# Optimization experiments

Measured on AMD Instinct MI355X. Metric: run time of the kernel, lower is better.

The kernel has to match this reference:

```python
import jax, jax.numpy as jnp
import numpy as np

KERNEL_MUL = 2.0
KERNEL_NUM = 5
EPS = 1e-3


def setup_inputs() -> dict:
    key = jax.random.key(0)
    k1, k2 = jax.random.split(key)
    source = jax.random.normal(k1, (2048, 512), dtype=jnp.float32)
    target = jax.random.normal(k2, (2048, 512), dtype=jnp.float32)
    beta = jnp.ones((KERNEL_NUM,), dtype=jnp.float32) / KERNEL_NUM
    return {"source": source, "target": target, "beta": beta}


def _sq_dists(total):
    # squared Euclidean pairwise distances, (N, N), clamped >= 0 (matches cdist(p=2)**2)
    sq = jnp.sum(total * total, axis=-1)
    d = sq[:, None] + sq[None, :] - 2.0 * (total @ total.T)
    return jnp.maximum(d, 0.0)


def _project_simplex(v):
    m = v.shape[0]
    mu = -jnp.sort(-v)                      # descending
    cs = jnp.cumsum(mu)
    ar = jnp.arange(1, m + 1, dtype=v.dtype)
    cond = mu - (cs - 1.0) / ar > 0
    idx = jnp.where(cond, jnp.arange(m), -1)
    rho = jnp.where(jnp.any(cond), jnp.max(idx), 0)
    theta = (cs[rho] - 1.0) / (rho + 1).astype(v.dtype)
    p = jnp.maximum(v - theta, 0.0)
    return p / (p.sum() + 1e-12)


def _update_beta(source, target, beta):
    # Batched version of the per-pair quad-kernel loop in _update_beta.
    Ns, D = source.shape
    Nt = target.shape[0]
    P = min(Ns // 2, Nt // 2)  # num_effective_pairs (static)
    s = source[: 2 * P].reshape(P, 2, D)
    t = target[: 2 * P].reshape(P, 2, D)
    quad = jnp.concatenate([s, t], axis=1)              # (P, 4, D) -> [s1, s2, t1, t2]
    diff = quad[:, :, None, :] - quad[:, None, :, :]
    sq = jnp.sum(diff * diff, axis=-1)                  # (P, 4, 4)
    offdiag = ~np.eye(4, dtype=bool)
    bw = jnp.median(sq[:, offdiag], axis=1) + 1e-6      # per-pair median of nonzero dists
    bw = bw / (KERNEL_MUL ** (KERNEL_NUM // 2))
    bws = bw[:, None] * (KERNEL_MUL ** jnp.arange(KERNEL_NUM, dtype=bw.dtype))[None, :]
    K = jnp.exp(-sq[:, None, :, :] / bws[:, :, None, None])   # (P, 5, 4, 4)
    g = K[:, :, 0, 1] + K[:, :, 2, 3] - K[:, :, 0, 2] - K[:, :, 1, 3]  # (P, 5)
    gm = jnp.mean(g, axis=0)
    Q = (g.T @ g) / P - jnp.outer(gm, gm) + EPS * jnp.eye(KERNEL_NUM, dtype=g.dtype)
    # projected gradient descent on the simplex (lr=1, max_iter=100, tol=1e-6)
    def cond_fn(st):
        _, _, i, conv = st
        return (i < 100) & (~conv)
    def body_fn(st):
        b, _, i, _ = st
        proj = _project_simplex(b - Q @ b)
        conv = jnp.linalg.norm(proj - b) < 1e-6
        return (proj, proj, i + 1, conv)
    _, proj, _, _ = jax.lax.while_loop(
        cond_fn, body_fn, (beta, beta, jnp.int32(0), jnp.array(False)))
    return proj


def _forward(source, target, beta):
    beta_new = _update_beta(jax.lax.stop_gradient(source),
                            jax.lax.stop_gradient(target), beta)
    Ns = source.shape[0]
    total = jnp.concatenate([source, target], axis=0)   # (N, D)
    N = total.shape[0]
    sq = _sq_dists(total)                               # (N, N)
    offdiag = ~np.eye(N, dtype=bool)
    bw = jnp.median(sq[offdiag]) + 1e-6
    bw = bw / (KERNEL_MUL ** (KERNEL_NUM // 2))
    bws = bw * (KERNEL_MUL ** jnp.arange(KERNEL_NUM, dtype=sq.dtype))  # (5,)
    Ks = jnp.exp(-sq[None, :, :] / bws[:, None, None])  # (5, N, N)
    joint = jnp.einsum('k,kij->ij', beta_new, Ks)
    XX = joint[:Ns, :Ns]
    YY = joint[Ns:, Ns:]
    XY = joint[:Ns, Ns:]
    n = XX.shape[0]
    m = YY.shape[0]
    term_XX = (jnp.sum(XX) - jnp.trace(XX)) / (n * (n - 1))
    term_YY = (jnp.sum(YY) - jnp.trace(YY)) / (m * (m - 1))
    term_XY = jnp.sum(XY) / (n * m)
    loss = term_XX + term_YY - 2.0 * term_XY
    return jnp.maximum(loss, 0.0)


def reference(source, target, beta):
    return _forward(source, target, beta)
```

## Files before the change

### kernel.cpp

```cpp
#include <hip/hip_runtime.h>
#include <math.h>

#define NT 4096
#define NS 2048
#define DDIM 512
#define KN 5
#define NTILES 528

typedef __bf16 bf16x8 __attribute__((ext_vector_type(8)));
typedef float f32x4 __attribute__((ext_vector_type(4)));
typedef unsigned short u16x8 __attribute__((ext_vector_type(8)));

static __device__ inline unsigned short f2bf(float x) {
    unsigned u = __float_as_uint(x);
    unsigned r = (u + 0x7fffu + ((u >> 16) & 1u)) >> 16;
    return (unsigned short)r;
}
static __device__ inline float bf2f(unsigned short h) {
    return __uint_as_float(((unsigned)h) << 16);
}

static __device__ inline void tri_map(int b, int& bx, int& by) {
    int x = (int)((sqrtf(8.0f * (float)b + 1.0f) - 1.0f) * 0.5f);
    while ((x + 1) * (x + 2) / 2 <= b) ++x;
    while (x * (x + 1) / 2 > b) --x;
    bx = x;
    by = b - x * (x + 1) / 2;
}

static __device__ void beta_solve(const float* __restrict__ g,
                                  const float* __restrict__ beta_in,
                                  float* __restrict__ beta_out)
{
    int lane = threadIdx.x;
    float gs[KN] = {0, 0, 0, 0, 0};
    float gg[15];
    #pragma unroll
    for (int i = 0; i < 15; ++i) gg[i] = 0.0f;
    for (int p = lane; p < 1024; p += 64) {
        float gv[KN];
        #pragma unroll
        for (int k = 0; k < KN; ++k) gv[k] = g[(size_t)p * KN + k];
        int idx = 0;
        #pragma unroll
        for (int a2 = 0; a2 < KN; ++a2) {
            gs[a2] += gv[a2];
            #pragma unroll
            for (int b2 = a2; b2 < KN; ++b2) gg[idx++] += gv[a2] * gv[b2];
        }
    }
    #pragma unroll
    for (int m = 32; m > 0; m >>= 1) {
        #pragma unroll
        for (int k = 0; k < KN; ++k) gs[k] += __shfl_xor(gs[k], m);
        #pragma unroll
        for (int i = 0; i < 15; ++i) gg[i] += __shfl_xor(gg[i], m);
    }
    if (lane != 0) return;

    float Q[KN][KN], gm[KN];
    #pragma unroll
    for (int k = 0; k < KN; ++k) gm[k] = gs[k] * (1.0f / 1024.0f);
    int idx = 0;
    #pragma unroll
    for (int a2 = 0; a2 < KN; ++a2)
        #pragma unroll
        for (int b2 = a2; b2 < KN; ++b2) {
            float qv = gg[idx++] * (1.0f / 1024.0f) - gm[a2] * gm[b2];
            Q[a2][b2] = qv; Q[b2][a2] = qv;
        }
    #pragma unroll
    for (int k = 0; k < KN; ++k) Q[k][k] += 0.001f;

    float b[KN], proj[KN];
    #pragma unroll
    for (int k = 0; k < KN; ++k) { b[k] = beta_in[k]; proj[k] = b[k]; }
    for (int it = 0; it < 100; ++it) {
        float v[KN];
        #pragma unroll
        for (int a2 = 0; a2 < KN; ++a2) {
            float qb = Q[a2][0] * b[0] + Q[a2][1] * b[1] + Q[a2][2] * b[2]
                     + Q[a2][3] * b[3] + Q[a2][4] * b[4];
            v[a2] = b[a2] - qb;
        }
        float mu0 = v[0], mu1 = v[1], mu2 = v[2], mu3 = v[3], mu4 = v[4];
#define CMPSW(x, y) { float hi_ = fmaxf(x, y); float lo_ = fminf(x, y); x = hi_; y = lo_; }
        CMPSW(mu0, mu1) CMPSW(mu3, mu4) CMPSW(mu2, mu4) CMPSW(mu2, mu3)
        CMPSW(mu0, mu3) CMPSW(mu0, mu2) CMPSW(mu1, mu4) CMPSW(mu1, mu3) CMPSW(mu1, mu2)
#undef CMPSW
        float cs0 = mu0, cs1 = cs0 + mu1, cs2 = cs1 + mu2, cs3 = cs2 + mu3, cs4 = cs3 + mu4;
        bool c1 = mu1 * 2.0f > cs1 - 1.0f;
        bool c2 = mu2 * 3.0f > cs2 - 1.0f;
        bool c3 = mu3 * 4.0f > cs3 - 1.0f;
        bool c4 = mu4 * 5.0f > cs4 - 1.0f;
        float csSel = cs0, rcpSel = 1.0f;
        if (c1) { csSel = cs1; rcpSel = 0.5f; }
        if (c2) { csSel = cs2; rcpSel = (1.0f / 3.0f); }
        if (c3) { csSel = cs3; rcpSel = 0.25f; }
        if (c4) { csSel = cs4; rcpSel = 0.2f; }
        float theta = (csSel - 1.0f) * rcpSel;
        float ssum = 0.0f;
        #pragma unroll
        for (int k = 0; k < KN; ++k) { proj[k] = fmaxf(v[k] - theta, 0.0f); ssum += proj[k]; }
        float invs = 1.0f / (ssum + 1e-12f);
        float nd = 0.0f;
        #pragma unroll
        for (int k = 0; k < KN; ++k) {
            proj[k] *= invs;
            float dd = proj[k] - b[k];
            nd += dd * dd;
            b[k] = proj[k];
        }
        if (nd < 1e-12f) break;
    }
    #pragma unroll
    for (int k = 0; k < KN; ++k) beta_out[k] = proj[k];
}

#define NZERO (4096 + 64 + 64 + 65536 + 65536)
__global__ __launch_bounds__(256) void k_prep2(const float* __restrict__ S,
                                               const float* __restrict__ T,
                                               unsigned short* __restrict__ Hi,
                                               unsigned short* __restrict__ Lo,
                                               float* __restrict__ norms,
                                               float* __restrict__ g,
                                               unsigned* __restrict__ hists,
                                               unsigned* __restrict__ sel)
{
    for (unsigned i = blockIdx.x * 256 + threadIdx.x; i < NZERO; i += 65536) hists[i] = 0;
    if (blockIdx.x == 50 && threadIdx.x == 0) {
        sel[0] = 0u; sel[1] = 8386559u;
        sel[2] = 0u; sel[3] = 8386560u;
    }
    int p = blockIdx.x * 4 + (threadIdx.x >> 6);
    int l = threadIdx.x & 63;
    const float* r0 = S + (size_t)(2 * p) * DDIM;
    const float* r1 = r0 + DDIM;
    const float* r2 = T + (size_t)(2 * p) * DDIM;
    const float* r3 = r2 + DDIM;
    float a[8], b[8], c[8], d[8];
    *(float4*)&a[0] = *(const float4*)(r0 + l * 8); *(float4*)&a[4] = *(const float4*)(r0 + l * 8 + 4);
    *(float4*)&b[0] = *(const float4*)(r1 + l * 8); *(float4*)&b[4] = *(const float4*)(r1 + l * 8 + 4);
    *(float4*)&c[0] = *(const float4*)(r2 + l * 8); *(float4*)&c[4] = *(const float4*)(r2 + l * 8 + 4);
    *(float4*)&d[0] = *(const float4*)(r3 + l * 8); *(float4*)&d[4] = *(const float4*)(r3 + l * 8 + 4);

    float n0 = 0, n1 = 0, n2 = 0, n3 = 0;
    float s01 = 0, s23 = 0, s02 = 0, s13 = 0, s03 = 0, s12 = 0;
    u16x8 h0, l0, h1, l1, h2, l2, h3, l3;
    #pragma unroll
    for (int k = 0; k < 8; ++k) {
        float va = a[k], vb = b[k], vc = c[k], vd = d[k];
        n0 += va * va; n1 += vb * vb; n2 += vc * vc; n3 += vd * vd;
        float t01 = va - vb, t23 = vc - vd, t02 = va - vc, t13 = vb - vd;
        s01 += t01*t01; s23 += t23*t23; s02 += t02*t02; s13 += t13*t13;
        float t03 = va - vd, t12 = vb - vc;
        s03 += t03*t03; s12 += t12*t12;
        unsigned short hh;
        hh = f2bf(va); h0[k] = hh; l0[k] = f2bf(va - bf2f(hh));
        hh = f2bf(vb); h1[k] = hh; l1[k] = f2bf(vb - bf2f(hh));
        hh = f2bf(vc); h2[k] = hh; l2[k] = f2bf(vc - bf2f(hh));
        hh = f2bf(vd); h3[k] = hh; l3[k] = f2bf(vd - bf2f(hh));
    }
    size_t g0 = (size_t)(2 * p) * DDIM + l * 8;
    size_t g1 = g0 + DDIM;
    size_t g2 = (size_t)(NS + 2 * p) * DDIM + l * 8;
    size_t g3 = g2 + DDIM;
    *(u16x8*)&Hi[g0] = h0; *(u16x8*)&Lo[g0] = l0;
    *(u16x8*)&Hi[g1] = h1; *(u16x8*)&Lo[g1] = l1;
    *(u16x8*)&Hi[g2] = h2; *(u16x8*)&Lo[g2] = l2;
    *(u16x8*)&Hi[g3] = h3; *(u16x8*)&Lo[g3] = l3;

    #pragma unroll
    for (int m = 32; m > 0; m >>= 1) {
        n0 += __shfl_xor(n0, m); n1 += __shfl_xor(n1, m);
        n2 += __shfl_xor(n2, m); n3 += __shfl_xor(n3, m);
        s01 += __shfl_xor(s01, m); s23 += __shfl_xor(s23, m);
        s02 += __shfl_xor(s02, m); s13 += __shfl_xor(s13, m);
        s03 += __shfl_xor(s03, m); s12 += __shfl_xor(s12, m);
    }
    if (l == 0) {
        norms[2 * p] = n0; norms[2 * p + 1] = n1;
        norms[NS + 2 * p] = n2; norms[NS + 2 * p + 1] = n3;
        float v[6] = { s01, s02, s03, s12, s13, s23 };
        for (int i = 0; i < 5; ++i)
            for (int j = 0; j < 5 - i; ++j)
                if (v[j] > v[j + 1]) { float t = v[j]; v[j] = v[j + 1]; v[j + 1] = t; }
        float med = 0.5f * (v[2] + v[3]);
        float bw = (med + 1e-6f) * 0.25f;
        #pragma unroll
        for (int k = 0; k < KN; ++k) {
            float inv = 1.0f / (bw * (float)(1 << k));
            g[(size_t)p * KN + k] = expf(-s01 * inv) + expf(-s23 * inv)
                                  - expf(-s02 * inv) - expf(-s13 * inv);
        }
    }
}

__global__ __launch_bounds__(256) void k_dist_mfma(const unsigned short* __restrict__ Hi,
                                                   const unsigned short* __restrict__ Lo,
                                                   const float* __restrict__ norms,
                                                   float* __restrict__ D,
                                                   unsigned short* __restrict__ D16,
                                                   int do16,
                                                   const float* __restrict__ g,
                                                   const float* __restrict__ beta_in,
                                                   float* __restrict__ beta_out)
{
    __shared__ __align__(16) unsigned short sA[2][2][128][32];
    __shared__ __align__(16) unsigned short sB[2][2][128][32];

    if (blockIdx.x == 0) {
        if (threadIdx.x < 64) beta_solve(g, beta_in, beta_out);
        return;
    }

    int bb = blockIdx.x - 1;
    int swz = (bb & 7) * 66 + (bb >> 3);
    int bx, by;
    tri_map(swz, bx, by);
    const int m0 = by * 128, n0 = bx * 128;

    const int tid = threadIdx.x;
    const int w = tid >> 6, l = tid & 63;
    const int wr = w >> 1, wc = w & 1;

    const int chunk = (l & 3) ^ ((((l >> 2) & 3) + ((l >> 4) & 3)) & 3);
    const size_t gA0 = (size_t)(m0 + w * 16 + (l >> 2)) * DDIM + chunk * 8;
    const size_t gA1 = gA0 + (size_t)64 * DDIM;
    const size_t gB0 = (size_t)(n0 + w * 16 + (l >> 2)) * DDIM + chunk * 8;
    const size_t gB1 = gB0 + (size_t)64 * DDIM;
    const unsigned w1024 = w * 1024;

#define GLD(dst, srcptr, goff)                                                      \
    __builtin_amdgcn_global_load_lds(                                               \
        (const __attribute__((address_space(1))) unsigned*)((srcptr) + (goff)),     \
        (__attribute__((address_space(3))) unsigned*)((char*)(dst) + w1024), 16, 0, 0)
#define STAGE(buf, kk)                                  \
    do {                                                \
        GLD(&sA[buf][0][0][0],  Hi, gA0 + (kk));        \
        GLD(&sA[buf][0][64][0], Hi, gA1 + (kk));        \
        GLD(&sA[buf][1][0][0],  Lo, gA0 + (kk));        \
        GLD(&sA[buf][1][64][0], Lo, gA1 + (kk));        \
        GLD(&sB[buf][0][0][0],  Hi, gB0 + (kk));        \
        GLD(&sB[buf][0][64][0], Hi, gB1 + (kk));        \
        GLD(&sB[buf][1][0][0],  Lo, gB0 + (kk));        \
        GLD(&sB[buf][1][64][0], Lo, gB1 + (kk));        \
    } while (0)

    f32x4 acc[4][4] = {};
    const int q = l >> 4;
    const int fr = ((l & 3) + ((l >> 2) & 3)) & 3;
    const unsigned soff = ((unsigned)(q ^ fr)) << 4;
    const unsigned rowbA = (wr * 64 + (l & 15)) * 64 + soff;
    const unsigned rowbB = (wc * 64 + (l & 15)) * 64 + soff;

    STAGE(0, 0);
    __syncthreads();

    #pragma unroll 2
    for (int t = 0; t < 16; ++t) {
        const int cur = t & 1;
        if (t < 15) STAGE(cur ^ 1, (t + 1) * 32);

        bf16x8 ah[4], al[4], bh[4], bl[4];
        #pragma unroll
        for (int m = 0; m < 4; ++m) {
            ah[m] = *(const bf16x8*)((const char*)&sA[cur][0][0][0] + rowbA + m * 1024);
            al[m] = *(const bf16x8*)((const char*)&sA[cur][1][0][0] + rowbA + m * 1024);
        }
        #pragma unroll
        for (int n = 0; n < 4; ++n) {
            bh[n] = *(const bf16x8*)((const char*)&sB[cur][0][0][0] + rowbB + n * 1024);
            bl[n] = *(const bf16x8*)((const char*)&sB[cur][1][0][0] + rowbB + n * 1024);
        }
        #pragma unroll
        for (int m = 0; m < 4; ++m)
            #pragma unroll
            for (int n = 0; n < 4; ++n) {
                acc[m][n] = __builtin_amdgcn_mfma_f32_16x16x32_bf16(bh[n], ah[m], acc[m][n], 0, 0, 0);
                acc[m][n] = __builtin_amdgcn_mfma_f32_16x16x32_bf16(bl[n], ah[m], acc[m][n], 0, 0, 0);
                acc[m][n] = __builtin_amdgcn_mfma_f32_16x16x32_bf16(bh[n], al[m], acc[m][n], 0, 0, 0);
            }
        __syncthreads();
    }
#undef STAGE
#undef GLD

    float* ncache = (float*)&sB[0][0][0][0];
    if (tid < 128) ncache[tid] = norms[m0 + tid];
    else           ncache[tid] = norms[n0 + tid - 128];
    __syncthreads();

    float* rowbuf = (float*)&sA[0][0][0][0] + w * 1024;
    const int rr = l & 15;
    #pragma unroll
    for (int m = 0; m < 4; ++m) {
        float nrm = ncache[wr * 64 + m * 16 + rr];
        #pragma unroll
        for (int n = 0; n < 4; ++n) {
            float4 ncv = *(const float4*)&ncache[128 + wc * 64 + n * 16 + (q << 2)];
            f32x4 a = acc[m][n];
            float4 o;
            o.x = fmaxf(nrm + ncv.x - 2.0f * a[0], 0.0f);
            o.y = fmaxf(nrm + ncv.y - 2.0f * a[1], 0.0f);
            o.z = fmaxf(nrm + ncv.z - 2.0f * a[2], 0.0f);
            o.w = fmaxf(nrm + ncv.w - 2.0f * a[3], 0.0f);
            int ch = (n * 4 + q) ^ (rr & 7);
            *(float4*)(rowbuf + rr * 64 + ch * 4) = o;
        }
        #pragma unroll
        for (int s = 0; s < 4; ++s) {
            int row = s * 4 + q;
            int ch = (l & 15) ^ (row & 7);
            float4 v = *(const float4*)(rowbuf + row * 64 + ch * 4);
            size_t base = (size_t)(m0 + wr * 64 + m * 16 + row) * NT + n0 + wc * 64 + (l & 15) * 4;
            *(float4*)&D[base] = v;
            if (do16) {
                ushort4 u;
                u.x = (unsigned short)(__float_as_uint(v.x) >> 16);
                u.y = (unsigned short)(__float_as_uint(v.y) >> 16);
                u.z = (unsigned short)(__float_as_uint(v.z) >> 16);
                u.w = (unsigned short)(__float_as_uint(v.w) >> 16);
                *(ushort4*)&D16[base] = u;
            }
        }
    }
}

template<bool S16>
__global__ __launch_bounds__(256) void k_h0(const float* __restrict__ D,
                                            const unsigned short* __restrict__ D16,
                                            unsigned* __restrict__ gH)
{
    __shared__ unsigned h[4096];
    for (int i = threadIdx.x; i < 4096; i += 256) h[i] = 0;
    int bx, by;
    tri_map(blockIdx.x, bx, by);
    int m0 = by * 128, n0 = bx * 128;
    unsigned wt = (bx != by) ? 2u : 1u;
    __syncthreads();
    if constexpr (S16) {
        for (int v = threadIdx.x; v < 2048; v += 256) {
            int r = m0 + (v >> 4);
            int c0 = n0 + (v & 15) * 8;
            u16x8 dv = *(const u16x8*)&D16[(size_t)r * NT + c0];
            unsigned pb = (unsigned)dv[0] >> 4;
            unsigned pc = (r == c0) ? 0u : wt;
            #pragma unroll
            for (int j = 1; j < 8; ++j) {
                unsigned bj = (unsigned)dv[j] >> 4;
                unsigned cj = (r == c0 + j) ? 0u : wt;
                if (bj == pb) pc += cj;
                else { if (pc) atomicAdd(&h[pb], pc); pb = bj; pc = cj; }
            }
            if (pc) atomicAdd(&h[pb], pc);
        }
    } else {
        for (int v = threadIdx.x; v < 4096; v += 256) {
            int r = m0 + (v >> 5);
            int c0 = n0 + (v & 31) * 4;
            float4 dv = *(const float4*)&D[(size_t)r * NT + c0];
            const float* dd = (const float*)&dv;
            unsigned pb = __float_as_uint(dd[0]) >> 20;
            unsigned pc = (r == c0) ? 0u : wt;
            #pragma unroll
            for (int j = 1; j < 4; ++j) {
                unsigned bj = __float_as_uint(dd[j]) >> 20;
                unsigned cj = (r == c0 + j) ? 0u : wt;
                if (bj == pb) pc += cj;
                else { if (pc) atomicAdd(&h[pb], pc); pb = bj; pc = cj; }
            }
            if (pc) atomicAdd(&h[pb], pc);
        }
    }
    __syncthreads();
    for (int i = threadIdx.x; i < 4096; i += 256) {
        unsigned c = h[i];
        if (c) atomicAdd(&gH[i], c);
    }
}

__global__ __launch_bounds__(256) void k_s0(const unsigned* __restrict__ gH,
                                            unsigned* __restrict__ sel)
{
    __shared__ unsigned ls[256];
    __shared__ unsigned res[4];
    int tid = threadIdx.x;
    uint4 a0 = *(const uint4*)&gH[tid * 16 + 0];
    uint4 a1 = *(const uint4*)&gH[tid * 16 + 4];
    uint4 a2 = *(const uint4*)&gH[tid * 16 + 8];
    uint4 a3 = *(const uint4*)&gH[tid * 16 + 12];
    unsigned V[16] = { a0.x,a0.y,a0.z,a0.w, a1.x,a1.y,a1.z,a1.w,
                       a2.x,a2.y,a2.z,a2.w, a3.x,a3.y,a3.z,a3.w };
    unsigned s = 0;
    #pragma unroll
    for (int i = 0; i < 16; ++i) s += V[i];
    ls[tid] = s;
    __syncthreads();
    for (int off = 1; off < 256; off <<= 1) {
        unsigned y = (tid >= off) ? ls[tid - off] : 0u;
        __syncthreads();
        ls[tid] += y;
        __syncthreads();
    }
    unsigned incl = ls[tid], base = incl - s;
    for (int t = 0; t < 2; ++t) {
        unsigned r = sel[t * 2 + 1];
        if (r >= base && r < incl) {
            unsigned cum = base, bin = 0, rem = 0;
            bool found = false;
            #pragma unroll
            for (int i = 0; i < 16; ++i) {
                unsigned hv = V[i];
                if (!found && r < cum + hv) { bin = tid * 16 + i; rem = r - cum; found = true; }
                cum += hv;
            }
            res[t * 2] = bin; res[t * 2 + 1] = rem;
        }
    }
    __syncthreads();
    if (tid == 0) { sel[0] = res[0]; sel[1] = res[1]; sel[2] = res[2]; sel[3] = res[3]; }
}

template<bool S16>
__global__ __launch_bounds__(256) void k_h1(const float* __restrict__ D,
                                            const unsigned short* __restrict__ D16,
                                            const unsigned* __restrict__ sel,
                                            unsigned* __restrict__ gA,
                                            unsigned* __restrict__ gB)
{
    __shared__ unsigned ha[16], hb[16];
    if (threadIdx.x < 16) { ha[threadIdx.x] = 0; hb[threadIdx.x] = 0; }
    unsigned pA = sel[0], pB = sel[2];
    int bx, by;
    tri_map(blockIdx.x, bx, by);
    int m0 = by * 128, n0 = bx * 128;
    unsigned wt = (bx != by) ? 2u : 1u;
    __syncthreads();
    if constexpr (S16) {
        for (int v = threadIdx.x; v < 2048; v += 256) {
            int r = m0 + (v >> 4);
            int c0 = n0 + (v & 15) * 8;
            u16x8 dv = *(const u16x8*)&D16[(size_t)r * NT + c0];
            #pragma unroll
            for (int j = 0; j < 8; ++j) {
                if (r == c0 + j) continue;
                unsigned k16 = dv[j];
                if ((k16 >> 4) == pA) atomicAdd(&ha[k16 & 15], wt);
                if ((k16 >> 4) == pB) atomicAdd(&hb[k16 & 15], wt);
            }
        }
    } else {
        for (int v = threadIdx.x; v < 4096; v += 256) {
            int r = m0 + (v >> 5);
            int c0 = n0 + (v & 31) * 4;
            float4 dv = *(const float4*)&D[(size_t)r * NT + c0];
            const float* dd = (const float*)&dv;
            #pragma unroll
            for (int j = 0; j < 4; ++j) {
                if (r == c0 + j) continue;
                unsigned key = __float_as_uint(dd[j]);
                if ((key >> 20) == pA) atomicAdd(&ha[(key >> 16) & 15], wt);
                if ((key >> 20) == pB) atomicAdd(&hb[(key >> 16) & 15], wt);
            }
        }
    }
    __syncthreads();
    if (threadIdx.x < 16) {
        unsigned ca = ha[threadIdx.x];
        if (ca) atomicAdd(&gA[threadIdx.x], ca);
        unsigned cb = hb[threadIdx.x];
        if (cb) atomicAdd(&gB[threadIdx.x], cb);
    }
}

__global__ __launch_bounds__(64) void k_s1(const unsigned* __restrict__ gA,
                                           const unsigned* __restrict__ gB,
                                           unsigned* __restrict__ sel)
{
    int lane = threadIdx.x;
    for (int t = 0; t < 2; ++t) {
        const unsigned* h = (t == 0) ? gA : gB;
        unsigned r = sel[t * 2 + 1];
        unsigned c = (lane < 16) ? h[lane] : 0u;
        unsigned x = c;
        #pragma unroll
        for (int off = 1; off < 16; off <<= 1) {
            unsigned y = __shfl_up(x, off);
            if (lane >= off) x += y;
        }
        unsigned base = x - c;
        if (lane < 16 && r >= base && r < base + c) {
            sel[t * 2 + 0] = (sel[t * 2 + 0] << 4) | (unsigned)lane;
            sel[t * 2 + 1] = r - base;
        }
    }
}

__global__ __launch_bounds__(256) void k_h2(const float* __restrict__ D,
                                            const unsigned* __restrict__ sel,
                                            unsigned* __restrict__ HA,
                                            unsigned* __restrict__ HB)
{
    unsigned pA = sel[0], pB = sel[2];
    int bx, by;
    tri_map(blockIdx.x, bx, by);
    int m0 = by * 128, n0 = bx * 128;
    unsigned wt = (bx != by) ? 2u : 1u;
    for (int v = threadIdx.x; v < 4096; v += 256) {
        int r = m0 + (v >> 5);
        int c0 = n0 + (v & 31) * 4;
        float4 dv = *(const float4*)&D[(size_t)r * NT + c0];
        const float* dd = (const float*)&dv;
        #pragma unroll
        for (int j = 0; j < 4; ++j) {
            if (r == c0 + j) continue;
            unsigned key = __float_as_uint(dd[j]);
            if ((key >> 16) == pA) atomicAdd(&HA[key & 0xffffu], wt);
            if ((key >> 16) == pB) atomicAdd(&HB[key & 0xffffu], wt);
        }
    }
}

__global__ __launch_bounds__(256) void k_s2(const unsigned* __restrict__ HA,
                                            const unsigned* __restrict__ HB,
                                            unsigned* __restrict__ sel,
                                            float* __restrict__ params)
{
    __shared__ unsigned ls[256];
    __shared__ unsigned keys[2];
    int tid = threadIdx.x;
    for (int t = 0; t < 2; ++t) {
        const unsigned* h = (t == 0) ? HA : HB;
        unsigned r = sel[t * 2 + 1];
        unsigned s = 0;
        for (int i = 0; i < 64; ++i) {
            uint4 u = *(const uint4*)&h[tid * 256 + i * 4];
            s += u.x + u.y + u.z + u.w;
        }
        ls[tid] = s;
        __syncthreads();
        for (int off = 1; off < 256; off <<= 1) {
            unsigned y = (tid >= off) ? ls[tid - off] : 0u;
            __syncthreads();
            ls[tid] += y;
            __syncthreads();
        }
        unsigned incl = ls[tid], base = incl - s;
        if (r >= base && r < incl) {
            unsigned cum = base;
            unsigned bin = 0;
            for (int i = 0; i < 64 && cum <= r; ++i) {
                uint4 u = *(const uint4*)&h[tid * 256 + i * 4];
                unsigned uu[4] = { u.x, u.y, u.z, u.w };
                #pragma unroll
                for (int j = 0; j < 4; ++j) {
                    if (r < cum + uu[j]) { bin = tid * 256 + i * 4 + j; cum = r + 1; goto done; }
                    cum += uu[j];
                }
            }
        done:
            keys[t] = (sel[t * 2] << 16) | bin;
        }
        __syncthreads();
    }
    if (tid == 0) {
        float med = 0.5f * (__uint_as_float(keys[0]) + __uint_as_float(keys[1]));
        float bw = (med + 1e-6f) * 0.25f;
        #pragma unroll
        for (int k = 0; k < KN; ++k) params[k] = 1.0f / (bw * (float)(1 << k));
    }
}

__global__ __launch_bounds__(256) void k_wsum_tri(const float* __restrict__ D,
                                                  const float* __restrict__ params,
                                                  const float* __restrict__ beta,
                                                  double* __restrict__ partials)
{
    float i0 = params[0], i1 = params[1], i2 = params[2], i3 = params[3], i4 = params[4];
    float b0 = beta[0], b1 = beta[1], b2 = beta[2], b3 = beta[3], b4 = beta[4];
    const double wDiag = 1.0 / ((double)NS * (NS - 1));
    const double wOff = -1.0 / ((double)NS * NS);
    int bx, by;
    tri_map(blockIdx.x, bx, by);
    int m0 = by * 128, n0 = bx * 128;
    double wt = (bx != by) ? 2.0 : 1.0;
    double acc = 0.0;
    for (int v = threadIdx.x; v < 4096; v += 256) {
        int r = m0 + (v >> 5);
        int c0 = n0 + (v & 31) * 4;
        float4 dv = *(const float4*)&D[(size_t)r * NT + c0];
        const float* dd = (const float*)&dv;
        #pragma unroll
        for (int j = 0; j < 4; ++j) {
            int c = c0 + j;
            if (r == c) continue;
            float sq = dd[j];
            float val = b0 * __expf(-sq * i0) + b1 * __expf(-sq * i1) + b2 * __expf(-sq * i2)
                      + b3 * __expf(-sq * i3) + b4 * __expf(-sq * i4);
            bool same = (r < NS) == (c < NS);
            acc += (same ? wDiag : wOff) * (double)val;
        }
    }
    acc *= wt;
    __shared__ double red[256];
    red[threadIdx.x] = acc;
    __syncthreads();
    for (int off = 128; off > 0; off >>= 1) {
        if (threadIdx.x < off) red[threadIdx.x] += red[threadIdx.x + off];
        __syncthreads();
    }
    if (threadIdx.x == 0) partials[blockIdx.x] = red[0];
}

__global__ __launch_bounds__(256) void k_final(const double* __restrict__ partials,
                                               float* __restrict__ out, int count)
{
    double acc = 0;
    for (int i = threadIdx.x; i < count; i += 256) acc += partials[i];
    __shared__ double red[256];
    red[threadIdx.x] = acc;
    __syncthreads();
    for (int off = 128; off > 0; off >>= 1) {
        if (threadIdx.x < off) red[threadIdx.x] += red[threadIdx.x + off];
        __syncthreads();
    }
    if (threadIdx.x == 0) out[0] = (float)fmax(red[0], 0.0);
}

extern "C" void kernel_launch(void* const* d_in, const int* in_sizes, int n_in,
                              void* d_out, int out_size, void* d_ws, size_t ws_size,
                              hipStream_t stream)
{
    const float* S = (const float*)d_in[0];
    const float* T = (const float*)d_in[1];
    const float* beta = (const float*)d_in[2];
    float* out = (float*)d_out;

    float* D = (float*)d_ws;
    unsigned short* Hi = (unsigned short*)(D + (size_t)NT * NT);
    unsigned short* Lo = Hi + (size_t)NT * DDIM;
    float* norms = (float*)(Lo + (size_t)NT * DDIM);
    float* g = norms + NT;
    float* beta2 = g + 1024 * KN;
    float* params = beta2 + 8;
    unsigned* sel = (unsigned*)(params + 8);
    unsigned* hists = sel + 16;
    unsigned* hL0 = hists;
    unsigned* h1A = hists + 4096;
    unsigned* h1B = hists + 4160;
    unsigned* HA  = hists + 4224;
    unsigned* HB  = HA + 65536;
    double* partials = (double*)(HB + 65536);
    unsigned short* D16 = (unsigned short*)(partials + NTILES);

    size_t need16 = (size_t)((char*)(D16 + (size_t)NT * NT) - (char*)d_ws);
    int do16 = (ws_size >= need16) ? 1 : 0;

    k_prep2<<<dim3(256), dim3(256), 0, stream>>>(S, T, Hi, Lo, norms, g, hists, sel);
    k_dist_mfma<<<dim3(NTILES + 1), dim3(256), 0, stream>>>(Hi, Lo, norms, D, D16, do16,
                                                            g, beta, beta2);
    if (do16) {
        k_h0<true><<<dim3(NTILES), dim3(256), 0, stream>>>(D, D16, hL0);
    } else {
        k_h0<false><<<dim3(NTILES), dim3(256), 0, stream>>>(D, D16, hL0);
    }
    k_s0<<<dim3(1), dim3(256), 0, stream>>>(hL0, sel);
    if (do16) {
        k_h1<true><<<dim3(NTILES), dim3(256), 0, stream>>>(D, D16, sel, h1A, h1B);
    } else {
        k_h1<false><<<dim3(NTILES), dim3(256), 0, stream>>>(D, D16, sel, h1A, h1B);
    }
    k_s1<<<dim3(1), dim3(64), 0, stream>>>(h1A, h1B, sel);
    k_h2<<<dim3(NTILES), dim3(256), 0, stream>>>(D, sel, HA, HB);
    k_s2<<<dim3(1), dim3(256), 0, stream>>>(HA, HB, sel, params);
    k_wsum_tri<<<dim3(NTILES), dim3(256), 0, stream>>>(D, params, beta2, partials);
    k_final<<<dim3(1), dim3(256), 0, stream>>>(partials, out, NTILES);
}
```

Baseline: 169.8 us.

## Fuse level-0 histogram into distance GEMM, deepen prefetch, fold final reduction

```diff
diff --git a/kernel.cpp b/kernel.cpp
--- a/kernel.cpp
+++ b/kernel.cpp
@@ -117,7 +117,7 @@
     for (int k = 0; k < KN; ++k) beta_out[k] = proj[k];
 }
 
-#define NZERO (4096 + 64 + 64 + 65536 + 65536)
+#define NZERO (4096 + 64 + 64 + 65536 + 65536 + 16)
 __global__ __launch_bounds__(256) void k_prep2(const float* __restrict__ S,
                                                const float* __restrict__ T,
                                                unsigned short* __restrict__ Hi,
@@ -204,7 +204,8 @@
                                                    int do16,
                                                    const float* __restrict__ g,
                                                    const float* __restrict__ beta_in,
-                                                   float* __restrict__ beta_out)
+                                                   float* __restrict__ beta_out,
+                                                   unsigned* __restrict__ gH)
 {
     __shared__ __align__(16) unsigned short sA[2][2][128][32];
     __shared__ __align__(16) unsigned short sB[2][2][128][32];
@@ -255,12 +256,14 @@
     const unsigned rowbB = (wc * 64 + (l & 15)) * 64 + soff;
 
     STAGE(0, 0);
-    __syncthreads();
+    STAGE(1, 32);
 
     #pragma unroll 2
     for (int t = 0; t < 16; ++t) {
         const int cur = t & 1;
-        if (t < 15) STAGE(cur ^ 1, (t + 1) * 32);
+        if (t < 15) { asm volatile("s_waitcnt vmcnt(8)" ::: "memory"); }
+        else        { asm volatile("s_waitcnt vmcnt(0)" ::: "memory"); }
+        __builtin_amdgcn_s_barrier();
 
         bf16x8 ah[4], al[4], bh[4], bl[4];
         #pragma unroll
@@ -273,6 +276,11 @@
             bh[n] = *(const bf16x8*)((const char*)&sB[cur][0][0][0] + rowbB + n * 1024);
             bl[n] = *(const bf16x8*)((const char*)&sB[cur][1][0][0] + rowbB + n * 1024);
         }
+        asm volatile("s_waitcnt lgkmcnt(0)" ::: "memory");
+        __builtin_amdgcn_s_barrier();
+        if (t < 14) STAGE(cur, (t + 2) * 32);
+        __builtin_amdgcn_sched_barrier(0);
+
         #pragma unroll
         for (int m = 0; m < 4; ++m)
             #pragma unroll
@@ -281,17 +289,20 @@
                 acc[m][n] = __builtin_amdgcn_mfma_f32_16x16x32_bf16(bl[n], ah[m], acc[m][n], 0, 0, 0);
                 acc[m][n] = __builtin_amdgcn_mfma_f32_16x16x32_bf16(bh[n], al[m], acc[m][n], 0, 0, 0);
             }
-        __syncthreads();
     }
 #undef STAGE
 #undef GLD
 
-    float* ncache = (float*)&sB[0][0][0][0];
+    unsigned* hrep = (unsigned*)&sB[0][0][0][0];
+    for (int i = tid; i < 8192; i += 256) hrep[i] = 0;
+    float* ncache = (float*)&sA[0][0][0][0];
     if (tid < 128) ncache[tid] = norms[m0 + tid];
     else           ncache[tid] = norms[n0 + tid - 128];
     __syncthreads();
 
-    float* rowbuf = (float*)&sA[0][0][0][0] + w * 1024;
+    unsigned* hmine = hrep + (w & 1) * 4096;
+    float* rowbuf = (float*)&sA[0][0][0][0] + 256 + w * 1024;
+    const unsigned wgt = (bx != by) ? 2u : 1u;
     const int rr = l & 15;
     #pragma unroll
     for (int m = 0; m < 4; ++m) {
@@ -313,7 +324,9 @@
             int row = s * 4 + q;
             int ch = (l & 15) ^ (row & 7);
             float4 v = *(const float4*)(rowbuf + row * 64 + ch * 4);
-            size_t base = (size_t)(m0 + wr * 64 + m * 16 + row) * NT + n0 + wc * 64 + (l & 15) * 4;
+            int rowg = m0 + wr * 64 + m * 16 + row;
+            int colg = n0 + wc * 64 + (l & 15) * 4;
+            size_t base = (size_t)rowg * NT + colg;
             *(float4*)&D[base] = v;
             if (do16) {
                 ushort4 u;
@@ -323,59 +336,24 @@
                 u.w = (unsigned short)(__float_as_uint(v.w) >> 16);
                 *(ushort4*)&D16[base] = u;
             }
-        }
-    }
-}
-
-template<bool S16>
-__global__ __launch_bounds__(256) void k_h0(const float* __restrict__ D,
-                                            const unsigned short* __restrict__ D16,
-                                            unsigned* __restrict__ gH)
-{
-    __shared__ unsigned h[4096];
-    for (int i = threadIdx.x; i < 4096; i += 256) h[i] = 0;
-    int bx, by;
-    tri_map(blockIdx.x, bx, by);
-    int m0 = by * 128, n0 = bx * 128;
-    unsigned wt = (bx != by) ? 2u : 1u;
-    __syncthreads();
-    if constexpr (S16) {
-        for (int v = threadIdx.x; v < 2048; v += 256) {
-            int r = m0 + (v >> 4);
-            int c0 = n0 + (v & 15) * 8;
-            u16x8 dv = *(const u16x8*)&D16[(size_t)r * NT + c0];
-            unsigned pb = (unsigned)dv[0] >> 4;
-            unsigned pc = (r == c0) ? 0u : wt;
-            #pragma unroll
-            for (int j = 1; j < 8; ++j) {
-                unsigned bj = (unsigned)dv[j] >> 4;
-                unsigned cj = (r == c0 + j) ? 0u : wt;
-                if (bj == pb) pc += cj;
-                else { if (pc) atomicAdd(&h[pb], pc); pb = bj; pc = cj; }
-            }
-            if (pc) atomicAdd(&h[pb], pc);
-        }
-    } else {
-        for (int v = threadIdx.x; v < 4096; v += 256) {
-            int r = m0 + (v >> 5);
-            int c0 = n0 + (v & 31) * 4;
-            float4 dv = *(const float4*)&D[(size_t)r * NT + c0];
-            const float* dd = (const float*)&dv;
-            unsigned pb = __float_as_uint(dd[0]) >> 20;
-            unsigned pc = (r == c0) ? 0u : wt;
-            #pragma unroll
-            for (int j = 1; j < 4; ++j) {
-                unsigned bj = __float_as_uint(dd[j]) >> 20;
-                unsigned cj = (r == c0 + j) ? 0u : wt;
-                if (bj == pb) pc += cj;
-                else { if (pc) atomicAdd(&h[pb], pc); pb = bj; pc = cj; }
-            }
-            if (pc) atomicAdd(&h[pb], pc);
-        }
-    }
-    __syncthreads();
-    for (int i = threadIdx.x; i < 4096; i += 256) {
-        unsigned c = h[i];
+            unsigned b0_ = __float_as_uint(v.x) >> 20;
+            unsigned b1_ = __float_as_uint(v.y) >> 20;
+            unsigned b2_ = __float_as_uint(v.z) >> 20;
+            unsigned b3_ = __float_as_uint(v.w) >> 20;
+            unsigned pb = b0_, pc = (rowg == colg) ? 0u : wgt;
+            unsigned cj;
+            cj = (rowg == colg + 1) ? 0u : wgt;
+            if (b1_ == pb) pc += cj; else { if (pc) atomicAdd(&hmine[pb], pc); pb = b1_; pc = cj; }
+            cj = (rowg == colg + 2) ? 0u : wgt;
+            if (b2_ == pb) pc += cj; else { if (pc) atomicAdd(&hmine[pb], pc); pb = b2_; pc = cj; }
+            cj = (rowg == colg + 3) ? 0u : wgt;
+            if (b3_ == pb) pc += cj; else { if (pc) atomicAdd(&hmine[pb], pc); pb = b3_; pc = cj; }
+            if (pc) atomicAdd(&hmine[pb], pc);
+        }
+    }
+    __syncthreads();
+    for (int i = tid; i < 4096; i += 256) {
+        unsigned c = hrep[i] + hrep[i + 4096];
         if (c) atomicAdd(&gH[i], c);
     }
 }
@@ -572,11 +550,15 @@
     }
 }
 
-__global__ __launch_bounds__(256) void k_wsum_tri(const float* __restrict__ D,
-                                                  const float* __restrict__ params,
-                                                  const float* __restrict__ beta,
-                                                  double* __restrict__ partials)
-{
+__global__ __launch_bounds__(256) void k_wsumf(const float* __restrict__ D,
+                                               const float* __restrict__ params,
+                                               const float* __restrict__ beta,
+                                               double* __restrict__ partials,
+                                               unsigned* __restrict__ cnt,
+                                               float* __restrict__ out)
+{
+    __shared__ double red[256];
+    __shared__ unsigned tk;
     float i0 = params[0], i1 = params[1], i2 = params[2], i3 = params[3], i4 = params[4];
     float b0 = beta[0], b1 = beta[1], b2 = beta[2], b3 = beta[3], b4 = beta[4];
     const double wDiag = 1.0 / ((double)NS * (NS - 1));
@@ -603,29 +585,33 @@
         }
     }
     acc *= wt;
-    __shared__ double red[256];
     red[threadIdx.x] = acc;
     __syncthreads();
     for (int off = 128; off > 0; off >>= 1) {
         if (threadIdx.x < off) red[threadIdx.x] += red[threadIdx.x + off];
         __syncthreads();
     }
-    if (threadIdx.x == 0) partials[blockIdx.x] = red[0];
-}
-
-__global__ __launch_bounds__(256) void k_final(const double* __restrict__ partials,
-                                               float* __restrict__ out, int count)
-{
-    double acc = 0;
-    for (int i = threadIdx.x; i < count; i += 256) acc += partials[i];
-    __shared__ double red[256];
-    red[threadIdx.x] = acc;
-    __syncthreads();
-    for (int off = 128; off > 0; off >>= 1) {
-        if (threadIdx.x < off) red[threadIdx.x] += red[threadIdx.x + off];
+    if (threadIdx.x == 0) {
+        partials[blockIdx.x] = red[0];
+        __threadfence();
+        tk = atomicAdd(&cnt[0], 1u);
+    }
+    __syncthreads();
+    if (tk == NTILES - 1) {
+        __threadfence();
+        double a2 = 0.0;
+        for (int i = threadIdx.x; i < NTILES; i += 256) {
+            unsigned long long u = atomicAdd((unsigned long long*)&partials[i], 0ull);
+            a2 += __longlong_as_double(u);
+        }
+        red[threadIdx.x] = a2;
         __syncthreads();
-    }
-    if (threadIdx.x == 0) out[0] = (float)fmax(red[0], 0.0);
+        for (int off = 128; off > 0; off >>= 1) {
+            if (threadIdx.x < off) red[threadIdx.x] += red[threadIdx.x + off];
+            __syncthreads();
+        }
+        if (threadIdx.x == 0) out[0] = (float)fmax(red[0], 0.0);
+    }
 }
 
 extern "C" void kernel_launch(void* const* d_in, const int* in_sizes, int n_in,
@@ -651,7 +637,8 @@
     unsigned* h1B = hists + 4160;
     unsigned* HA  = hists + 4224;
     unsigned* HB  = HA + 65536;
-    double* partials = (double*)(HB + 65536);
+    unsigned* cnt = hists + 135296;
+    double* partials = (double*)(hists + 135312);
     unsigned short* D16 = (unsigned short*)(partials + NTILES);
 
     size_t need16 = (size_t)((char*)(D16 + (size_t)NT * NT) - (char*)d_ws);
@@ -659,12 +646,7 @@
 
     k_prep2<<<dim3(256), dim3(256), 0, stream>>>(S, T, Hi, Lo, norms, g, hists, sel);
     k_dist_mfma<<<dim3(NTILES + 1), dim3(256), 0, stream>>>(Hi, Lo, norms, D, D16, do16,
-                                                            g, beta, beta2);
-    if (do16) {
-        k_h0<true><<<dim3(NTILES), dim3(256), 0, stream>>>(D, D16, hL0);
-    } else {
-        k_h0<false><<<dim3(NTILES), dim3(256), 0, stream>>>(D, D16, hL0);
-    }
+                                                            g, beta, beta2, hL0);
     k_s0<<<dim3(1), dim3(256), 0, stream>>>(hL0, sel);
     if (do16) {
         k_h1<true><<<dim3(NTILES), dim3(256), 0, stream>>>(D, D16, sel, h1A, h1B);
@@ -674,6 +656,5 @@
     k_s1<<<dim3(1), dim3(64), 0, stream>>>(h1A, h1B, sel);
     k_h2<<<dim3(NTILES), dim3(256), 0, stream>>>(D, sel, HA, HB);
     k_s2<<<dim3(1), dim3(256), 0, stream>>>(HA, HB, sel, params);
-    k_wsum_tri<<<dim3(NTILES), dim3(256), 0, stream>>>(D, params, beta2, partials);
-    k_final<<<dim3(1), dim3(256), 0, stream>>>(partials, out, NTILES);
-}
+    k_wsumf<<<dim3(NTILES), dim3(256), 0, stream>>>(D, params, beta2, partials, cnt, out);
+}
```

Result: slower. 173.7 us (+2.3%).
